# Optimization experiments

Measured on AMD Instinct MI355X. Metric: run time of the kernel, lower is better.

The kernel has to match this reference:

```python
import jax, jax.numpy as jnp
import numpy as np

EPS = 1e-10
FAR_DELTA = 1e10  # delta appended for the last sample, as in the torch code


def setup_inputs() -> dict:
    key = jax.random.key(0)
    k1, k2, k3 = jax.random.split(key, 3)
    N, P, C = 131072, 128, 3
    density = jax.random.normal(k1, (N, P), dtype=jnp.float32)  # raw density (relu'd inside)
    feature = jax.random.uniform(k2, (N, P, C), dtype=jnp.float32)
    # depth values must be increasing along the sample dim (they come from a ray sampler);
    # build them as a cumulative sum of positive steps in roughly [0, 6].
    steps = jax.random.uniform(k3, (N, P), dtype=jnp.float32) * 0.05
    depth_values = jnp.cumsum(steps, axis=-1) + 1.0
    return {"density": density, "feature": feature, "depth_values": depth_values}


def reference(density, feature, depth_values):
    # deltas: consecutive depth differences, huge delta for the final sample  [N, P]
    deltas = jnp.concatenate(
        [depth_values[:, 1:] - depth_values[:, :-1],
         jnp.full_like(depth_values[:, :1], FAR_DELTA)], axis=-1)
    # alpha = 1 - exp(-relu(density) * delta)   [N, P]
    alpha = 1.0 - jnp.exp(-jax.nn.relu(density) * deltas)
    # transmittance: exclusive cumprod of (1 - alpha + eps)   [N, P]
    trans = jnp.cumprod(
        jnp.concatenate([jnp.ones_like(alpha[:, :1]), 1.0 - alpha + EPS], axis=-1),
        axis=-1)[:, :-1]
    weights = alpha * trans  # [N, P]
    feat_out = jnp.sum(weights[..., None] * feature, axis=1)  # [N, C]
    depth_out = jnp.sum(weights * depth_values, axis=1)       # [N]
    return feat_out, depth_out
```

## Files before the change

kernel.cpp:

```cpp
#include <hip/hip_runtime.h>

#define EPS 1e-10f
#define FAR_DELTA 1e10f

__global__ __launch_bounds__(256) void volrend_kernel(
    const float* __restrict__ density,
    const float* __restrict__ feature,
    const float* __restrict__ depth,
    float* __restrict__ feat_out,
    float* __restrict__ depth_out,
    int N)
{
    const int tid  = threadIdx.x;
    const int lane = tid & 63;
    const int wv   = tid >> 6;
    const int j    = lane & 15;
    const int sub  = lane >> 4;
    const int ray  = blockIdx.x * 16 + wv * 4 + sub;
    if (ray >= N) return;

    const float4* d4 = (const float4*)(density + (size_t)ray * 128 + j * 8);
    const float4* z4 = (const float4*)(depth   + (size_t)ray * 128 + j * 8);
    const float4* f4 = (const float4*)(feature + (size_t)ray * 384 + j * 24);

    float4 dA = d4[0], dB = d4[1];
    float4 zA = z4[0], zB = z4[1];

    float z[8]  = {zA.x, zA.y, zA.z, zA.w, zB.x, zB.y, zB.z, zB.w};
    float dn[8] = {dA.x, dA.y, dA.z, dA.w, dB.x, dB.y, dB.z, dB.w};

    float znext = __shfl_down(z[0], 1, 64);

    float al[8], tt[8];
    #pragma unroll
    for (int k = 0; k < 8; ++k) {
        float delta = (k < 7) ? (z[k + 1] - z[k])
                              : ((j == 15) ? FAR_DELTA : (znext - z[7]));
        float ex = __expf(-fmaxf(dn[k], 0.0f) * delta);
        al[k] = 1.0f - ex;
        tt[k] = ex + EPS;
    }

    float loc = tt[0];
    #pragma unroll
    for (int k = 1; k < 8; ++k) loc *= tt[k];

    float s = loc;
    #pragma unroll
    for (int off = 1; off < 16; off <<= 1) {
        float v = __shfl_up(s, off, 16);
        if (j >= off) s *= v;
    }
    float excl = __shfl_up(s, 1, 16);
    if (j == 0) excl = 1.0f;

    float4 F0 = f4[0], F1 = f4[1], F2 = f4[2], F3 = f4[3], F4 = f4[4], F5 = f4[5];
    float f[24] = {F0.x, F0.y, F0.z, F0.w, F1.x, F1.y, F1.z, F1.w,
                   F2.x, F2.y, F2.z, F2.w, F3.x, F3.y, F3.z, F3.w,
                   F4.x, F4.y, F4.z, F4.w, F5.x, F5.y, F5.z, F5.w};

    float trans = excl;
    float a0 = 0.0f, a1 = 0.0f, a2 = 0.0f, ad = 0.0f;
    #pragma unroll
    for (int k = 0; k < 8; ++k) {
        float wk = al[k] * trans;
        trans *= tt[k];
        a0 += wk * f[3 * k + 0];
        a1 += wk * f[3 * k + 1];
        a2 += wk * f[3 * k + 2];
        ad += wk * z[k];
    }

    #pragma unroll
    for (int off = 8; off >= 1; off >>= 1) {
        a0 += __shfl_xor(a0, off, 16);
        a1 += __shfl_xor(a1, off, 16);
        a2 += __shfl_xor(a2, off, 16);
        ad += __shfl_xor(ad, off, 16);
    }

    if (j == 0) {
        feat_out[(size_t)ray * 3 + 0] = a0;
        feat_out[(size_t)ray * 3 + 1] = a1;
        feat_out[(size_t)ray * 3 + 2] = a2;
        depth_out[ray] = ad;
    }
}

extern "C" void kernel_launch(void* const* d_in, const int* in_sizes, int n_in,
                              void* d_out, int out_size, void* d_ws, size_t ws_size,
                              hipStream_t stream) {
    const float* density = (const float*)d_in[0];
    const float* feature = (const float*)d_in[1];
    const float* depth   = (const float*)d_in[2];

    const int P = 128;
    const int N = in_sizes[0] / P;

    float* feat_out  = (float*)d_out;
    float* depth_out = (float*)d_out + (size_t)N * 3;

    dim3 grid((N + 15) / 16);
    dim3 block(256);
    volrend_kernel<<<grid, block, 0, stream>>>(density, feature, depth,
                                               feat_out, depth_out, N);
}
```

Measured before the change: 349.2 us.

## Stage feature loads through LDS with async global_load_lds and factor out exclusive transmittance

Feature data for each wave's four rays is now copied into shared memory with the asynchronous global_load_lds builtin, issued before the transmittance math, so the load overlaps with the exp and scan work and global reads are fully coalesced. Weights are computed once against a local transmittance and scaled by the exclusive prefix at the end, which removes the second multiply chain. Launch bounds now request 8 blocks per CU. The change adds 24KB of LDS per block, which may cap occupancy, and a __syncthreads placed after an early return, which is a risk for partial blocks.

```diff
diff --git a/kernel.cpp b/kernel.cpp
--- a/kernel.cpp
+++ b/kernel.cpp
@@ -3,7 +3,7 @@
 #define EPS 1e-10f
 #define FAR_DELTA 1e10f
 
-__global__ __launch_bounds__(256) void volrend_kernel(
+__global__ __launch_bounds__(256, 8) void volrend_kernel(
     const float* __restrict__ density,
     const float* __restrict__ feature,
     const float* __restrict__ depth,
@@ -11,41 +11,54 @@
     float* __restrict__ depth_out,
     int N)
 {
+    __shared__ __align__(16) float featLDS[4 * 1536];
+
     const int tid  = threadIdx.x;
     const int lane = tid & 63;
     const int wv   = tid >> 6;
     const int j    = lane & 15;
     const int sub  = lane >> 4;
-    const int ray  = blockIdx.x * 16 + wv * 4 + sub;
+    const int r0   = blockIdx.x * 16 + wv * 4;
+    const int ray  = r0 + sub;
     if (ray >= N) return;
 
     const float4* d4 = (const float4*)(density + (size_t)ray * 128 + j * 8);
     const float4* z4 = (const float4*)(depth   + (size_t)ray * 128 + j * 8);
-    const float4* f4 = (const float4*)(feature + (size_t)ray * 384 + j * 24);
-
     float4 dA = d4[0], dB = d4[1];
     float4 zA = z4[0], zB = z4[1];
+
+    {
+        const char* gb = (const char*)(feature + (size_t)r0 * 384) + lane * 16;
+        char*       lb = (char*)&featLDS[wv * 1536];
+        #pragma unroll
+        for (int i = 0; i < 6; ++i) {
+            __builtin_amdgcn_global_load_lds(
+                (const __attribute__((address_space(1))) void*)(gb + i * 1024),
+                (__attribute__((address_space(3))) void*)(lb + i * 1024),
+                16, 0, 0);
+        }
+    }
 
     float z[8]  = {zA.x, zA.y, zA.z, zA.w, zB.x, zB.y, zB.z, zB.w};
     float dn[8] = {dA.x, dA.y, dA.z, dA.w, dB.x, dB.y, dB.z, dB.w};
 
     float znext = __shfl_down(z[0], 1, 64);
 
-    float al[8], tt[8];
+    float wl[8];
+    float tl  = 1.0f;
+    float adP = 0.0f;
     #pragma unroll
     for (int k = 0; k < 8; ++k) {
         float delta = (k < 7) ? (z[k + 1] - z[k])
                               : ((j == 15) ? FAR_DELTA : (znext - z[7]));
         float ex = __expf(-fmaxf(dn[k], 0.0f) * delta);
-        al[k] = 1.0f - ex;
-        tt[k] = ex + EPS;
+        float tk = ex + EPS;
+        wl[k] = (1.0f - ex) * tl;
+        adP  += wl[k] * z[k];
+        tl   *= tk;
     }
 
-    float loc = tt[0];
-    #pragma unroll
-    for (int k = 1; k < 8; ++k) loc *= tt[k];
-
-    float s = loc;
+    float s = tl;
     #pragma unroll
     for (int off = 1; off < 16; off <<= 1) {
         float v = __shfl_up(s, off, 16);
@@ -54,22 +67,24 @@
     float excl = __shfl_up(s, 1, 16);
     if (j == 0) excl = 1.0f;
 
-    float4 F0 = f4[0], F1 = f4[1], F2 = f4[2], F3 = f4[3], F4 = f4[4], F5 = f4[5];
+    __syncthreads();
+
+    const float4* fl = (const float4*)&featLDS[wv * 1536 + sub * 384 + j * 24];
+    float4 F0 = fl[0], F1 = fl[1], F2 = fl[2], F3 = fl[3], F4 = fl[4], F5 = fl[5];
     float f[24] = {F0.x, F0.y, F0.z, F0.w, F1.x, F1.y, F1.z, F1.w,
                    F2.x, F2.y, F2.z, F2.w, F3.x, F3.y, F3.z, F3.w,
                    F4.x, F4.y, F4.z, F4.w, F5.x, F5.y, F5.z, F5.w};
 
-    float trans = excl;
-    float a0 = 0.0f, a1 = 0.0f, a2 = 0.0f, ad = 0.0f;
+    float a0 = 0.0f, a1 = 0.0f, a2 = 0.0f;
     #pragma unroll
     for (int k = 0; k < 8; ++k) {
-        float wk = al[k] * trans;
-        trans *= tt[k];
-        a0 += wk * f[3 * k + 0];
-        a1 += wk * f[3 * k + 1];
-        a2 += wk * f[3 * k + 2];
-        ad += wk * z[k];
+        a0 += wl[k] * f[3 * k + 0];
+        a1 += wl[k] * f[3 * k + 1];
+        a2 += wl[k] * f[3 * k + 2];
     }
+
+    a0 *= excl; a1 *= excl; a2 *= excl;
+    float ad = adP * excl;
 
     #pragma unroll
     for (int off = 8; off >= 1; off >>= 1) {
```

Result: no change. 353.7 us (+1.3%).

## Process one ray per thread with register double-buffered sequential scan

Applied to the files above, without the earlier changes.

Replaces the 16-lanes-per-ray design, which used a warp-shuffle prefix product, with one thread per ray. Each thread walks the 128 samples in chunks of 8 and prefetches the next chunk into registers. Density is read with nontemporal loads. This removes the shuffle scan and reductions, but makes each thread's loads strided across lanes, lengthens the serial dependency chain, and cuts the number of waves available to hide memory latency.

```diff
diff --git a/kernel.cpp b/kernel.cpp
--- a/kernel.cpp
+++ b/kernel.cpp
@@ -2,6 +2,8 @@
 
 #define EPS 1e-10f
 #define FAR_DELTA 1e10f
+
+typedef float f32x4 __attribute__((ext_vector_type(4)));
 
 __global__ __launch_bounds__(256) void volrend_kernel(
     const float* __restrict__ density,
@@ -11,80 +13,60 @@
     float* __restrict__ depth_out,
     int N)
 {
-    const int tid  = threadIdx.x;
-    const int lane = tid & 63;
-    const int wv   = tid >> 6;
-    const int j    = lane & 15;
-    const int sub  = lane >> 4;
-    const int ray  = blockIdx.x * 16 + wv * 4 + sub;
+    const int ray = blockIdx.x * 256 + threadIdx.x;
     if (ray >= N) return;
 
-    const float4* d4 = (const float4*)(density + (size_t)ray * 128 + j * 8);
-    const float4* z4 = (const float4*)(depth   + (size_t)ray * 128 + j * 8);
-    const float4* f4 = (const float4*)(feature + (size_t)ray * 384 + j * 24);
+    const f32x4* d4 = (const f32x4*)(density + (size_t)ray * 128);
+    const f32x4* z4 = (const f32x4*)(depth   + (size_t)ray * 128);
+    const f32x4* f4 = (const f32x4*)(feature + (size_t)ray * 384);
 
-    float4 dA = d4[0], dB = d4[1];
-    float4 zA = z4[0], zB = z4[1];
+    f32x4 cd0, cd1, cz0, cz1, cf0, cf1, cf2, cf3, cf4, cf5;
+    f32x4 nd0, nd1, nz0, nz1, nf0, nf1, nf2, nf3, nf4, nf5;
 
-    float z[8]  = {zA.x, zA.y, zA.z, zA.w, zB.x, zB.y, zB.z, zB.w};
-    float dn[8] = {dA.x, dA.y, dA.z, dA.w, dB.x, dB.y, dB.z, dB.w};
+    cd0 = __builtin_nontemporal_load(&d4[0]);
+    cd1 = __builtin_nontemporal_load(&d4[1]);
+    cz0 = z4[0]; cz1 = z4[1];
+    cf0 = f4[0]; cf1 = f4[1]; cf2 = f4[2]; cf3 = f4[3]; cf4 = f4[4]; cf5 = f4[5];
 
-    float znext = __shfl_down(z[0], 1, 64);
+    float trans = 1.0f;
+    float a0 = 0.0f, a1 = 0.0f, a2 = 0.0f, ad = 0.0f;
 
-    float al[8], tt[8];
     #pragma unroll
-    for (int k = 0; k < 8; ++k) {
-        float delta = (k < 7) ? (z[k + 1] - z[k])
-                              : ((j == 15) ? FAR_DELTA : (znext - z[7]));
-        float ex = __expf(-fmaxf(dn[k], 0.0f) * delta);
-        al[k] = 1.0f - ex;
-        tt[k] = ex + EPS;
+    for (int b = 0; b < 16; ++b) {
+        const int bn = (b < 15) ? (b + 1) : 15;
+        nd0 = __builtin_nontemporal_load(&d4[bn * 2 + 0]);
+        nd1 = __builtin_nontemporal_load(&d4[bn * 2 + 1]);
+        nz0 = z4[bn * 2 + 0]; nz1 = z4[bn * 2 + 1];
+        nf0 = f4[bn * 6 + 0]; nf1 = f4[bn * 6 + 1]; nf2 = f4[bn * 6 + 2];
+        nf3 = f4[bn * 6 + 3]; nf4 = f4[bn * 6 + 4]; nf5 = f4[bn * 6 + 5];
+
+        float z[9]  = {cz0.x, cz0.y, cz0.z, cz0.w, cz1.x, cz1.y, cz1.z, cz1.w,
+                       nz0.x};
+        float dn[8] = {cd0.x, cd0.y, cd0.z, cd0.w, cd1.x, cd1.y, cd1.z, cd1.w};
+        float f[24] = {cf0.x, cf0.y, cf0.z, cf0.w, cf1.x, cf1.y, cf1.z, cf1.w,
+                       cf2.x, cf2.y, cf2.z, cf2.w, cf3.x, cf3.y, cf3.z, cf3.w,
+                       cf4.x, cf4.y, cf4.z, cf4.w, cf5.x, cf5.y, cf5.z, cf5.w};
+
+        #pragma unroll
+        for (int k = 0; k < 8; ++k) {
+            float delta = (b == 15 && k == 7) ? FAR_DELTA : (z[k + 1] - z[k]);
+            float ex = __expf(-fmaxf(dn[k], 0.0f) * delta);
+            float wk = (1.0f - ex) * trans;
+            trans *= (ex + EPS);
+            a0 += wk * f[3 * k + 0];
+            a1 += wk * f[3 * k + 1];
+            a2 += wk * f[3 * k + 2];
+            ad += wk * z[k];
+        }
+
+        cd0 = nd0; cd1 = nd1; cz0 = nz0; cz1 = nz1;
+        cf0 = nf0; cf1 = nf1; cf2 = nf2; cf3 = nf3; cf4 = nf4; cf5 = nf5;
     }
 
-    float loc = tt[0];
-    #pragma unroll
-    for (int k = 1; k < 8; ++k) loc *= tt[k];
-
-    float s = loc;
-    #pragma unroll
-    for (int off = 1; off < 16; off <<= 1) {
-        float v = __shfl_up(s, off, 16);
-        if (j >= off) s *= v;
-    }
-    float excl = __shfl_up(s, 1, 16);
-    if (j == 0) excl = 1.0f;
-
-    float4 F0 = f4[0], F1 = f4[1], F2 = f4[2], F3 = f4[3], F4 = f4[4], F5 = f4[5];
-    float f[24] = {F0.x, F0.y, F0.z, F0.w, F1.x, F1.y, F1.z, F1.w,
-                   F2.x, F2.y, F2.z, F2.w, F3.x, F3.y, F3.z, F3.w,
-                   F4.x, F4.y, F4.z, F4.w, F5.x, F5.y, F5.z, F5.w};
-
-    float trans = excl;
-    float a0 = 0.0f, a1 = 0.0f, a2 = 0.0f, ad = 0.0f;
-    #pragma unroll
-    for (int k = 0; k < 8; ++k) {
-        float wk = al[k] * trans;
-        trans *= tt[k];
-        a0 += wk * f[3 * k + 0];
-        a1 += wk * f[3 * k + 1];
-        a2 += wk * f[3 * k + 2];
-        ad += wk * z[k];
-    }
-
-    #pragma unroll
-    for (int off = 8; off >= 1; off >>= 1) {
-        a0 += __shfl_xor(a0, off, 16);
-        a1 += __shfl_xor(a1, off, 16);
-        a2 += __shfl_xor(a2, off, 16);
-        ad += __shfl_xor(ad, off, 16);
-    }
-
-    if (j == 0) {
-        feat_out[(size_t)ray * 3 + 0] = a0;
-        feat_out[(size_t)ray * 3 + 1] = a1;
-        feat_out[(size_t)ray * 3 + 2] = a2;
-        depth_out[ray] = ad;
-    }
+    feat_out[(size_t)ray * 3 + 0] = a0;
+    feat_out[(size_t)ray * 3 + 1] = a1;
+    feat_out[(size_t)ray * 3 + 2] = a2;
+    depth_out[ray] = ad;
 }
 
 extern "C" void kernel_launch(void* const* d_in, const int* in_sizes, int n_in,
@@ -100,7 +82,7 @@
     float* feat_out  = (float*)d_out;
     float* depth_out = (float*)d_out + (size_t)N * 3;
 
-    dim3 grid((N + 15) / 16);
+    dim3 grid((N + 255) / 256);
     dim3 block(256);
     volrend_kernel<<<grid, block, 0, stream>>>(density, feature, depth,
                                                feat_out, depth_out, N);
```

Result: slower. 433.1 us (+24.0%).
